# Kernel tuning notes

Measured on AMD Instinct MI355X. Metric: run time of the kernel, lower is better.

The kernel has to match this reference:

```python
import jax, jax.numpy as jnp
import numpy as np

EMBED_DIM = 2048
NUM_HEADS = 32
NUM_KV_HEADS = 8
HEAD_DIM = EMBED_DIM // NUM_HEADS  # 64
KV_DIM = NUM_KV_HEADS * HEAD_DIM   # 512


def setup_inputs() -> dict:
    key = jax.random.key(0)
    ks = jax.random.split(key, 5)
    B, S = 2, 2048
    scale = 0.02
    x = jax.random.normal(ks[0], (B, S, EMBED_DIM), dtype=jnp.float32)
    Wq = jax.random.normal(ks[1], (EMBED_DIM, EMBED_DIM), dtype=jnp.float32) * scale
    Wk = jax.random.normal(ks[2], (EMBED_DIM, KV_DIM), dtype=jnp.float32) * scale
    Wv = jax.random.normal(ks[3], (EMBED_DIM, KV_DIM), dtype=jnp.float32) * scale
    Wo = jax.random.normal(ks[4], (EMBED_DIM, EMBED_DIM), dtype=jnp.float32) * scale
    return {"x": x, "Wq": Wq, "Wk": Wk, "Wv": Wv, "Wo": Wo}


def reference(x, Wq, Wk, Wv, Wo):
    B, S, _ = x.shape
    g = NUM_HEADS // NUM_KV_HEADS  # queries per kv head
    # projections -> [B, H, S, D]
    q = (x @ Wq).reshape(B, S, NUM_HEADS, HEAD_DIM).transpose(0, 2, 1, 3)
    k = (x @ Wk).reshape(B, S, NUM_KV_HEADS, HEAD_DIM).transpose(0, 2, 1, 3)
    v = (x @ Wv).reshape(B, S, NUM_KV_HEADS, HEAD_DIM).transpose(0, 2, 1, 3)
    # GQA repeat_interleave on head dim
    k = jnp.repeat(k, g, axis=1)
    v = jnp.repeat(v, g, axis=1)
    scores = jnp.einsum('bhqd,bhkd->bhqk', q, k) / np.sqrt(HEAD_DIM).astype(np.float32)
    causal = jnp.tril(jnp.ones((S, S), dtype=bool))
    scores = jnp.where(causal, scores, jnp.finfo(x.dtype).min)
    attn = jax.nn.softmax(scores, axis=-1)
    out = jnp.einsum('bhqk,bhkd->bhqd', attn, v)  # [B, H, S, D]
    out = out.transpose(0, 2, 1, 3).reshape(B, S, EMBED_DIM)
    return out @ Wo
```

## Files before the change

### kernel.cpp

```cpp
#include <hip/hip_runtime.h>
#include <hip/hip_bf16.h>
#include <cstdint>
#include <type_traits>

#define EMBED 2048
#define SLEN 2048
#define NB 2
#define NHEADS 32
#define HDIM 64
#define KVDIM 512
#define MTOT (NB * SLEN)
#define NQKV (EMBED + 2 * KVDIM)

typedef __attribute__((ext_vector_type(8))) __bf16 bf16x8;
typedef __attribute__((ext_vector_type(4))) float f32x4;
typedef __attribute__((ext_vector_type(16))) float f32x16;

#define QSCALE 0.18033688011112042f

__device__ __forceinline__ ushort f2bf(float f) {
    union { float f; uint32_t u; } v; v.f = f;
    uint32_t r = (v.u + 0x7FFFu + ((v.u >> 16) & 1u)) >> 16;
    return (ushort)r;
}

__device__ __forceinline__ void gload_lds16(const ushort* g, ushort* l) {
    __builtin_amdgcn_global_load_lds(
        (const __attribute__((address_space(1))) void*)g,
        (__attribute__((address_space(3))) void*)l, 16, 0, 0);
}

__global__ __launch_bounds__(256) void k_prep(const float* __restrict__ x,
                                              const float* __restrict__ Wq,
                                              const float* __restrict__ Wk,
                                              const float* __restrict__ Wv,
                                              const float* __restrict__ Wo,
                                              ushort* __restrict__ xb,
                                              ushort* __restrict__ wt,
                                              ushort* __restrict__ wot) {
    const int tid = threadIdx.x;
    int bid = blockIdx.x;
    if (bid < 8192) {
        int i = bid * 256 + tid;
        float4 v = *(const float4*)(x + (size_t)i * 4);
        ushort4 o;
        o.x = f2bf(v.x); o.y = f2bf(v.y); o.z = f2bf(v.z); o.w = f2bf(v.w);
        *(ushort4*)(xb + (size_t)i * 4) = o;
        return;
    }
    bid -= 8192;
    const float* W; ushort* Wt; int N; float scale; int bx, by;
    if (bid < 4096)      { W = Wq; Wt = wt;                                   N = EMBED; scale = QSCALE; bx = bid & 63; by = bid >> 6; }
    else if (bid < 5120) { W = Wk; Wt = wt + (size_t)EMBED * EMBED;           N = KVDIM; scale = 1.f; int b2 = bid - 4096; bx = b2 & 15; by = b2 >> 4; }
    else if (bid < 6144) { W = Wv; Wt = wt + (size_t)(EMBED + KVDIM) * EMBED; N = KVDIM; scale = 1.f; int b2 = bid - 5120; bx = b2 & 15; by = b2 >> 4; }
    else                 { W = Wo; Wt = wot;                                  N = EMBED; scale = 1.f; int b2 = bid - 6144; bx = b2 & 63; by = b2 >> 6; }
    const int K = EMBED;
    __shared__ float tile[32][33];
    const int tx = tid & 31, ty = tid >> 5;
    const int xcol = bx * 32 + tx;
    const int y0 = by * 32;
    #pragma unroll
    for (int i = ty; i < 32; i += 8)
        tile[i][tx] = W[(size_t)(y0 + i) * N + xcol];
    __syncthreads();
    const int xo = y0 + tx;
    const int yo0 = bx * 32;
    #pragma unroll
    for (int i = ty; i < 32; i += 8)
        Wt[(size_t)(yo0 + i) * K + xo] = f2bf(tile[tx][i] * scale);
}

__global__ __launch_bounds__(256) void k_transpose_v(const ushort* __restrict__ V,
                                                     ushort* __restrict__ VT) {
    __shared__ ushort tile[64][65];
    const int tx = threadIdx.x, ty = threadIdx.y;
    const int x0 = blockIdx.x * 64;
    const int y0 = blockIdx.y * 64;
    #pragma unroll
    for (int i = ty; i < 64; i += 4)
        tile[i][tx] = V[(size_t)(y0 + i) * KVDIM + x0 + tx];
    __syncthreads();
    #pragma unroll
    for (int i = ty; i < 64; i += 4)
        VT[(size_t)(x0 + i) * MTOT + y0 + tx] = tile[tx][i];
}

__device__ __forceinline__ int2 xcd_swizzle(int gx, int gy) {
    const int nwg = gx * gy;
    int f = blockIdx.y * gx + blockIdx.x;
    const int cpx = nwg >> 3;
    f = (f & 7) * cpx + (f >> 3);
    return make_int2(f % gx, f / gx);
}

__global__ __launch_bounds__(256) void k_gemm_qkv(const ushort* __restrict__ A,
                                                  const ushort* __restrict__ Bt,
                                                  ushort* __restrict__ Qb,
                                                  ushort* __restrict__ Kb,
                                                  ushort* __restrict__ Vb) {
    __shared__ alignas(16) ushort As[2][128 * 32];
    __shared__ alignas(16) ushort Bs[2][128 * 32];

    const int tid = threadIdx.x;
    const int lane = tid & 63;
    const int w = tid >> 6;
    const int wr = w >> 1, wc = w & 1;
    const int l15 = lane & 15, g = lane >> 4;
    const int2 bxy = xcd_swizzle(NQKV / 128, MTOT / 128);
    const int n0 = bxy.x * 128;
    const int m0 = bxy.y * 128;
    const int K = EMBED;

    f32x4 acc[4][4] = {};

    const int c0 = tid, c1 = tid + 256;
    const int rA0 = c0 >> 2, sA0 = c0 & 3;
    const int rA1 = c1 >> 2, sA1 = c1 & 3;

    const ushort* pA0 = A + (size_t)(m0 + rA0) * K + sA0 * 8;
    const ushort* pA1 = A + (size_t)(m0 + rA1) * K + sA1 * 8;
    const ushort* pB0 = Bt + (size_t)(n0 + rA0) * K + sA0 * 8;
    const ushort* pB1 = Bt + (size_t)(n0 + rA1) * K + sA1 * 8;

    gload_lds16(pA0, &As[0][c0 * 8]);
    gload_lds16(pA1, &As[0][c1 * 8]);
    gload_lds16(pB0, &Bs[0][c0 * 8]);
    gload_lds16(pB1, &Bs[0][c1 * 8]);
    __syncthreads();

    int cur = 0;
    for (int k0 = 0; k0 < K; k0 += 32) {
        if (k0 + 32 < K) {
            gload_lds16(pA0 + k0 + 32, &As[cur ^ 1][c0 * 8]);
            gload_lds16(pA1 + k0 + 32, &As[cur ^ 1][c1 * 8]);
            gload_lds16(pB0 + k0 + 32, &Bs[cur ^ 1][c0 * 8]);
            gload_lds16(pB1 + k0 + 32, &Bs[cur ^ 1][c1 * 8]);
        }
        bf16x8 a[4], b[4];
        #pragma unroll
        for (int i = 0; i < 4; i++)
            a[i] = *(const bf16x8*)&As[cur][(wr * 64 + i * 16 + l15) * 32 + 8 * g];
        #pragma unroll
        for (int j = 0; j < 4; j++)
            b[j] = *(const bf16x8*)&Bs[cur][(wc * 64 + j * 16 + l15) * 32 + 8 * g];
        #pragma unroll
        for (int i = 0; i < 4; i++)
            #pragma unroll
            for (int j = 0; j < 4; j++)
                acc[i][j] = __builtin_amdgcn_mfma_f32_16x16x32_bf16(a[i], b[j], acc[i][j], 0, 0, 0);
        __syncthreads();
        cur ^= 1;
    }

    ushort* Cb; int Nout, cbase;
    if (n0 < EMBED)              { Cb = Qb; Nout = EMBED; cbase = n0; }
    else if (n0 < EMBED + KVDIM) { Cb = Kb; Nout = KVDIM; cbase = n0 - EMBED; }
    else                         { Cb = Vb; Nout = KVDIM; cbase = n0 - EMBED - KVDIM; }

    #pragma unroll
    for (int i = 0; i < 4; i++) {
        #pragma unroll
        for (int j = 0; j < 4; j++) {
            const int row = m0 + wr * 64 + i * 16 + g * 4;
            const int col = cbase + wc * 64 + j * 16 + l15;
            #pragma unroll
            for (int r = 0; r < 4; r++)
                Cb[(size_t)(row + r) * Nout + col] = f2bf(acc[i][j][r]);
        }
    }
}

template <typename OUT_T>
__global__ __launch_bounds__(256) void k_gemm_bt(const ushort* __restrict__ A,
                                                 const ushort* __restrict__ Bt,
                                                 OUT_T* __restrict__ C,
                                                 int M, int N, int K) {
    __shared__ alignas(16) ushort As[2][128 * 64];
    __shared__ alignas(16) ushort Bs[2][128 * 64];

    const int tid = threadIdx.x;
    const int lane = tid & 63;
    const int w = tid >> 6;
    const int wr = w >> 1, wc = w & 1;
    const int l15 = lane & 15, g = lane >> 4;
    const int2 bxy = xcd_swizzle(N / 128, M / 128);
    const int n0 = bxy.x * 128;
    const int m0 = bxy.y * 128;

    f32x4 acc[4][4] = {};

    const ushort* pA[4];
    const ushort* pB[4];
    #pragma unroll
    for (int t = 0; t < 4; t++) {
        const int c = tid + 256 * t;
        const int r = c >> 3, gr = c & 7;
        const int sg = gr ^ (r & 7);
        pA[t] = A + (size_t)(m0 + r) * K + sg * 8;
        pB[t] = Bt + (size_t)(n0 + r) * K + sg * 8;
    }

    #pragma unroll
    for (int t = 0; t < 4; t++) {
        gload_lds16(pA[t], &As[0][(tid + 256 * t) * 8]);
        gload_lds16(pB[t], &Bs[0][(tid + 256 * t) * 8]);
    }
    __syncthreads();

    int cur = 0;
    for (int k0 = 0; k0 < K; k0 += 64) {
        if (k0 + 64 < K) {
            #pragma unroll
            for (int t = 0; t < 4; t++) {
                gload_lds16(pA[t] + k0 + 64, &As[cur ^ 1][(tid + 256 * t) * 8]);
                gload_lds16(pB[t] + k0 + 64, &Bs[cur ^ 1][(tid + 256 * t) * 8]);
            }
        }
        #pragma unroll
        for (int kk = 0; kk < 2; kk++) {
            bf16x8 a[4], b[4];
            #pragma unroll
            for (int i = 0; i < 4; i++)
                a[i] = *(const bf16x8*)&As[cur][(wr * 64 + i * 16 + l15) * 64 +
                                                (((4 * kk + g) ^ (l15 & 7)) << 3)];
            #pragma unroll
            for (int j = 0; j < 4; j++)
                b[j] = *(const bf16x8*)&Bs[cur][(wc * 64 + j * 16 + l15) * 64 +
                                                (((4 * kk + g) ^ (l15 & 7)) << 3)];
            #pragma unroll
            for (int i = 0; i < 4; i++)
                #pragma unroll
                for (int j = 0; j < 4; j++)
                    acc[i][j] = __builtin_amdgcn_mfma_f32_16x16x32_bf16(a[i], b[j], acc[i][j], 0, 0, 0);
        }
        __syncthreads();
        cur ^= 1;
    }

    #pragma unroll
    for (int i = 0; i < 4; i++) {
        #pragma unroll
        for (int j = 0; j < 4; j++) {
            const int row = m0 + wr * 64 + i * 16 + g * 4;
            const int col = n0 + wc * 64 + j * 16 + l15;
            #pragma unroll
            for (int r = 0; r < 4; r++) {
                float val = acc[i][j][r];
                if constexpr (std::is_same<OUT_T, ushort>::value)
                    C[(size_t)(row + r) * N + col] = f2bf(val);
                else
                    C[(size_t)(row + r) * N + col] = val;
            }
        }
    }
}

__global__ __launch_bounds__(512, 4) void k_attn(const ushort* __restrict__ Qg,
                                                 const ushort* __restrict__ Kg,
                                                 const ushort* __restrict__ VTg,
                                                 ushort* __restrict__ Og) {
    __shared__ alignas(16) ushort Ks[2][64 * 64];
    __shared__ alignas(16) ushort Vs[2][64 * 64];

    const int tid = threadIdx.x;
    const int lane = tid & 63;
    const int wq = tid >> 6;
    const int l31 = lane & 31;
    const int hi = lane >> 5;

    const int flat = blockIdx.x + (blockIdx.y << 3) + (blockIdx.z << 8);
    const int lo = flat & 255, hv = flat >> 8;
    const int bi = hv ? (7 - (lo & 7)) : (lo & 7);
    const int h = lo >> 3;
    const int b = hv;
    const int kh = h >> 2;
    const size_t rowbase = (size_t)b * SLEN;

    const int q0 = bi * 256;
    const int qw0 = q0 + wq * 32;
    const int nt = (q0 >> 6) + 4;

    bf16x8 qf[4];
    {
        const ushort* qrow = Qg + (rowbase + qw0 + l31) * EMBED + h * HDIM;
        #pragma unroll
        for (int s = 0; s < 4; s++)
            qf[s] = *(const bf16x8*)(qrow + s * 16 + hi * 8);
    }

    const int srow = tid >> 3;
    const int sgr = tid & 7;
    const int woff = srow * 64 + ((sgr ^ (srow & 7)) << 3);
    const ushort* kgbase = Kg + (rowbase + srow) * KVDIM + kh * HDIM + sgr * 8;
    const ushort* vgbase = VTg + (size_t)(kh * HDIM + srow) * MTOT + b * SLEN + sgr * 8;

    {
        uint4 kr = *(const uint4*)kgbase;
        uint4 vr = *(const uint4*)vgbase;
        *(uint4*)&Ks[0][woff] = kr;
        *(uint4*)&Vs[0][woff] = vr;
    }
    __syncthreads();

    f32x16 oacc[2];
    #pragma unroll
    for (int d = 0; d < 2; d++)
        #pragma unroll
        for (int r = 0; r < 16; r++) oacc[d][r] = 0.f;
    float l_run = 0.f;

    int cur = 0;
    for (int kt = 0; kt < nt; ++kt) {
        const int k0 = kt * 64;
        const bool pref = (kt + 1 < nt);
        uint4 kr, vr;
        if (pref) {
            kr = *(const uint4*)(kgbase + (size_t)(k0 + 64) * KVDIM);
            vr = *(const uint4*)(vgbase + k0 + 64);
        }

        if (k0 <= qw0 + 31) {
            f32x16 sacc[2];
            #pragma unroll
            for (int st = 0; st < 2; st++)
                #pragma unroll
                for (int r = 0; r < 16; r++) sacc[st][r] = 0.f;
            __builtin_amdgcn_s_setprio(1);
            #pragma unroll
            for (int st = 0; st < 2; st++) {
                const int krow = st * 32 + l31;
                #pragma unroll
                for (int s = 0; s < 4; s++) {
                    bf16x8 af = *(const bf16x8*)&Ks[cur][krow * 64 + (((2 * s + hi) ^ (l31 & 7)) << 3)];
                    sacc[st] = __builtin_amdgcn_mfma_f32_32x32x16_bf16(af, qf[s], sacc[st], 0, 0, 0);
                }
            }
            __builtin_amdgcn_s_setprio(0);
            if (k0 + 63 > qw0) {
                const int q = qw0 + l31;
                #pragma unroll
                for (int st = 0; st < 2; st++)
                    #pragma unroll
                    for (int r = 0; r < 16; r++) {
                        int kpos = k0 + st * 32 + (r & 3) + 8 * (r >> 2) + 4 * hi;
                        if (kpos > q) sacc[st][r] = -1e30f;
                    }
            }
            float lsum = 0.f;
            #pragma unroll
            for (int st = 0; st < 2; st++)
                #pragma unroll
                for (int r = 0; r < 16; r++) {
                    float p = __builtin_amdgcn_exp2f(sacc[st][r]);
                    sacc[st][r] = p;
                    lsum += p;
                }
            lsum += __shfl_xor(lsum, 32);
            l_run += lsum;
            uint32_t pr[2][8];
            #pragma unroll
            for (int st = 0; st < 2; st++)
                #pragma unroll
                for (int k = 0; k < 8; k++) {
                    uint32_t d;
                    asm("v_cvt_pk_bf16_f32 %0, %1, %2"
                        : "=v"(d) : "v"(sacc[st][2 * k]), "v"(sacc[st][2 * k + 1]));
                    pr[st][k] = d;
                }
            #pragma unroll
            for (int c = 0; c < 2; c++) {
                #pragma unroll
                for (int tt = 0; tt < 2; tt++) {
                    const int pb = 4 * tt;
                    uint32_t w0 = pr[c][pb + 0], w2 = pr[c][pb + 2];
                    uint32_t w1 = pr[c][pb + 1], w3 = pr[c][pb + 3];
                    asm("v_permlane32_swap_b32 %0, %1" : "+v"(w0), "+v"(w2));
                    asm("v_permlane32_swap_b32 %0, %1" : "+v"(w1), "+v"(w3));
                    union { uint32_t u[4]; bf16x8 v; } pf;
                    pf.u[0] = w0; pf.u[1] = w1; pf.u[2] = w2; pf.u[3] = w3;
                    const int t = 2 * c + tt;
                    __builtin_amdgcn_s_setprio(1);
                    #pragma unroll
                    for (int dt = 0; dt < 2; dt++) {
                        const int vrow = dt * 32 + l31;
                        bf16x8 vf = *(const bf16x8*)&Vs[cur][vrow * 64 + (((2 * t + hi) ^ (l31 & 7)) << 3)];
                        oacc[dt] = __builtin_amdgcn_mfma_f32_32x32x16_bf16(pf.v, vf, oacc[dt], 0, 0, 0);
                    }
                    __builtin_amdgcn_s_setprio(0);
                }
            }
        }

        __syncthreads();
        if (pref) {
            *(uint4*)&Ks[cur ^ 1][woff] = kr;
            *(uint4*)&Vs[cur ^ 1][woff] = vr;
        }
        __syncthreads();
        cur ^= 1;
    }

    #pragma unroll
    for (int r = 0; r < 16; r++) {
        const int rr = (r & 3) + 8 * (r >> 2) + 4 * hi;
        float lr = __shfl(l_run, rr | (lane & 32));
        float inv = 1.f / lr;
        const size_t base = (rowbase + qw0 + rr) * EMBED + h * HDIM;
        Og[base + l31] = f2bf(oacc[0][r] * inv);
        Og[base + 32 + l31] = f2bf(oacc[1][r] * inv);
    }
}

#define WS_XB  ((size_t)0)
#define WS_QB  (WS_XB + (size_t)MTOT * EMBED)
#define WS_KB  (WS_QB + (size_t)MTOT * EMBED)
#define WS_VB  (WS_KB + (size_t)MTOT * KVDIM)
#define WS_WT  (WS_VB + (size_t)MTOT * KVDIM)
#define WS_WOT (WS_WT + (size_t)NQKV * EMBED)
#define WS_VT  WS_WT

extern "C" void kernel_launch(void* const* d_in, const int* in_sizes, int n_in,
                              void* d_out, int out_size, void* d_ws, size_t ws_size,
                              hipStream_t stream) {
    const float* x  = (const float*)d_in[0];
    const float* Wq = (const float*)d_in[1];
    const float* Wk = (const float*)d_in[2];
    const float* Wv = (const float*)d_in[3];
    const float* Wo = (const float*)d_in[4];
    float* out = (float*)d_out;
    ushort* ws = (ushort*)d_ws;

    k_prep<<<18432, 256, 0, stream>>>(x, Wq, Wk, Wv, Wo,
                                      ws + WS_XB, ws + WS_WT, ws + WS_WOT);

    k_gemm_qkv<<<dim3(NQKV / 128, MTOT / 128), 256, 0, stream>>>(
        ws + WS_XB, ws + WS_WT, ws + WS_QB, ws + WS_KB, ws + WS_VB);

    k_transpose_v<<<dim3(KVDIM / 64, MTOT / 64), dim3(64, 4), 0, stream>>>(
        ws + WS_VB, ws + WS_VT);

    k_attn<<<dim3(8, 32, 2), 512, 0, stream>>>(
        ws + WS_QB, ws + WS_KB, ws + WS_VT, ws + WS_XB);

    k_gemm_bt<float><<<dim3(EMBED / 128, MTOT / 128), 256, 0, stream>>>(
        ws + WS_XB, ws + WS_WOT, out, MTOT, EMBED, EMBED);
}
```

Baseline: 189.4 us.

## Split fused QKV GEMM into Q GEMM and a smaller-tile KV GEMM

Replaces the single QKV projection kernel (BK=32, 128x128 tiles) with two launches: the existing K=64-step bt GEMM for Q, and a new KV GEMM using 64x128 tiles with XOR-swizzled LDS and BK=64. K and V are written interleaved into one buffer with a 1024-element row stride, so the transpose and attention kernels now index through that stride. This aims to use the deeper-K, bank-conflict-free GEMM path and give the narrow KV projection more workgroups. The cost is an extra kernel launch and a less compact K layout for attention loads.

```diff
diff --git a/kernel.cpp b/kernel.cpp
--- a/kernel.cpp
+++ b/kernel.cpp
@@ -9,6 +9,7 @@
 #define NHEADS 32
 #define HDIM 64
 #define KVDIM 512
+#define KVSTRIDE 1024
 #define MTOT (NB * SLEN)
 #define NQKV (EMBED + 2 * KVDIM)
 
@@ -70,7 +71,7 @@
         Wt[(size_t)(yo0 + i) * K + xo] = f2bf(tile[tx][i] * scale);
 }
 
-__global__ __launch_bounds__(256) void k_transpose_v(const ushort* __restrict__ V,
+__global__ __launch_bounds__(256) void k_transpose_v(const ushort* __restrict__ KV,
                                                      ushort* __restrict__ VT) {
     __shared__ ushort tile[64][65];
     const int tx = threadIdx.x, ty = threadIdx.y;
@@ -78,7 +79,7 @@
     const int y0 = blockIdx.y * 64;
     #pragma unroll
     for (int i = ty; i < 64; i += 4)
-        tile[i][tx] = V[(size_t)(y0 + i) * KVDIM + x0 + tx];
+        tile[i][tx] = KV[(size_t)(y0 + i) * KVSTRIDE + KVDIM + x0 + tx];
     __syncthreads();
     #pragma unroll
     for (int i = ty; i < 64; i += 4)
@@ -91,83 +92,6 @@
     const int cpx = nwg >> 3;
     f = (f & 7) * cpx + (f >> 3);
     return make_int2(f % gx, f / gx);
-}
-
-__global__ __launch_bounds__(256) void k_gemm_qkv(const ushort* __restrict__ A,
-                                                  const ushort* __restrict__ Bt,
-                                                  ushort* __restrict__ Qb,
-                                                  ushort* __restrict__ Kb,
-                                                  ushort* __restrict__ Vb) {
-    __shared__ alignas(16) ushort As[2][128 * 32];
-    __shared__ alignas(16) ushort Bs[2][128 * 32];
-
-    const int tid = threadIdx.x;
-    const int lane = tid & 63;
-    const int w = tid >> 6;
-    const int wr = w >> 1, wc = w & 1;
-    const int l15 = lane & 15, g = lane >> 4;
-    const int2 bxy = xcd_swizzle(NQKV / 128, MTOT / 128);
-    const int n0 = bxy.x * 128;
-    const int m0 = bxy.y * 128;
-    const int K = EMBED;
-
-    f32x4 acc[4][4] = {};
-
-    const int c0 = tid, c1 = tid + 256;
-    const int rA0 = c0 >> 2, sA0 = c0 & 3;
-    const int rA1 = c1 >> 2, sA1 = c1 & 3;
-
-    const ushort* pA0 = A + (size_t)(m0 + rA0) * K + sA0 * 8;
-    const ushort* pA1 = A + (size_t)(m0 + rA1) * K + sA1 * 8;
-    const ushort* pB0 = Bt + (size_t)(n0 + rA0) * K + sA0 * 8;
-    const ushort* pB1 = Bt + (size_t)(n0 + rA1) * K + sA1 * 8;
-
-    gload_lds16(pA0, &As[0][c0 * 8]);
-    gload_lds16(pA1, &As[0][c1 * 8]);
-    gload_lds16(pB0, &Bs[0][c0 * 8]);
-    gload_lds16(pB1, &Bs[0][c1 * 8]);
-    __syncthreads();
-
-    int cur = 0;
-    for (int k0 = 0; k0 < K; k0 += 32) {
-        if (k0 + 32 < K) {
-            gload_lds16(pA0 + k0 + 32, &As[cur ^ 1][c0 * 8]);
-            gload_lds16(pA1 + k0 + 32, &As[cur ^ 1][c1 * 8]);
-            gload_lds16(pB0 + k0 + 32, &Bs[cur ^ 1][c0 * 8]);
-            gload_lds16(pB1 + k0 + 32, &Bs[cur ^ 1][c1 * 8]);
-        }
-        bf16x8 a[4], b[4];
-        #pragma unroll
-        for (int i = 0; i < 4; i++)
-            a[i] = *(const bf16x8*)&As[cur][(wr * 64 + i * 16 + l15) * 32 + 8 * g];
-        #pragma unroll
-        for (int j = 0; j < 4; j++)
-            b[j] = *(const bf16x8*)&Bs[cur][(wc * 64 + j * 16 + l15) * 32 + 8 * g];
-        #pragma unroll
-        for (int i = 0; i < 4; i++)
-            #pragma unroll
-            for (int j = 0; j < 4; j++)
-                acc[i][j] = __builtin_amdgcn_mfma_f32_16x16x32_bf16(a[i], b[j], acc[i][j], 0, 0, 0);
-        __syncthreads();
-        cur ^= 1;
-    }
-
-    ushort* Cb; int Nout, cbase;
-    if (n0 < EMBED)              { Cb = Qb; Nout = EMBED; cbase = n0; }
-    else if (n0 < EMBED + KVDIM) { Cb = Kb; Nout = KVDIM; cbase = n0 - EMBED; }
-    else                         { Cb = Vb; Nout = KVDIM; cbase = n0 - EMBED - KVDIM; }
-
-    #pragma unroll
-    for (int i = 0; i < 4; i++) {
-        #pragma unroll
-        for (int j = 0; j < 4; j++) {
-            const int row = m0 + wr * 64 + i * 16 + g * 4;
-            const int col = cbase + wc * 64 + j * 16 + l15;
-            #pragma unroll
-            for (int r = 0; r < 4; r++)
-                Cb[(size_t)(row + r) * Nout + col] = f2bf(acc[i][j][r]);
-        }
-    }
 }
 
 template <typename OUT_T>
@@ -255,8 +179,95 @@
     }
 }
 
+__global__ __launch_bounds__(256) void k_gemm_kv(const ushort* __restrict__ A,
+                                                 const ushort* __restrict__ Bt,
+                                                 ushort* __restrict__ C) {
+    __shared__ alignas(16) ushort As[2][64 * 64];
+    __shared__ alignas(16) ushort Bs[2][128 * 64];
+
+    const int tid = threadIdx.x;
+    const int lane = tid & 63;
+    const int w = tid >> 6;
+    const int wr = w >> 1, wc = w & 1;
+    const int l15 = lane & 15, g = lane >> 4;
+    const int2 bxy = xcd_swizzle(KVSTRIDE / 128, MTOT / 64);
+    const int n0 = bxy.x * 128;
+    const int m0 = bxy.y * 64;
+    const int K = EMBED;
+
+    f32x4 acc[2][4] = {};
+
+    const ushort* pA[2];
+    const ushort* pB[4];
+    #pragma unroll
+    for (int t = 0; t < 2; t++) {
+        const int c = tid + 256 * t;
+        const int r = c >> 3, gr = c & 7;
+        const int sg = gr ^ (r & 7);
+        pA[t] = A + (size_t)(m0 + r) * K + sg * 8;
+    }
+    #pragma unroll
+    for (int t = 0; t < 4; t++) {
+        const int c = tid + 256 * t;
+        const int r = c >> 3, gr = c & 7;
+        const int sg = gr ^ (r & 7);
+        pB[t] = Bt + (size_t)(n0 + r) * K + sg * 8;
+    }
+
+    #pragma unroll
+    for (int t = 0; t < 2; t++)
+        gload_lds16(pA[t], &As[0][(tid + 256 * t) * 8]);
+    #pragma unroll
+    for (int t = 0; t < 4; t++)
+        gload_lds16(pB[t], &Bs[0][(tid + 256 * t) * 8]);
+    __syncthreads();
+
+    int cur = 0;
+    for (int k0 = 0; k0 < K; k0 += 64) {
+        if (k0 + 64 < K) {
+            #pragma unroll
+            for (int t = 0; t < 2; t++)
+                gload_lds16(pA[t] + k0 + 64, &As[cur ^ 1][(tid + 256 * t) * 8]);
+            #pragma unroll
+            for (int t = 0; t < 4; t++)
+                gload_lds16(pB[t] + k0 + 64, &Bs[cur ^ 1][(tid + 256 * t) * 8]);
+        }
+        #pragma unroll
+        for (int kk = 0; kk < 2; kk++) {
+            bf16x8 a[2], b[4];
+            #pragma unroll
+            for (int i = 0; i < 2; i++)
+                a[i] = *(const bf16x8*)&As[cur][(wr * 32 + i * 16 + l15) * 64 +
+                                                (((4 * kk + g) ^ (l15 & 7)) << 3)];
+            #pragma unroll
+            for (int j = 0; j < 4; j++)
+                b[j] = *(const bf16x8*)&Bs[cur][(wc * 64 + j * 16 + l15) * 64 +
+                                                (((4 * kk + g) ^ (l15 & 7)) << 3)];
+            #pragma unroll
+            for (int i = 0; i < 2; i++)
+                #pragma unroll
+                for (int j = 0; j < 4; j++)
+                    acc[i][j] = __builtin_amdgcn_mfma_f32_16x16x32_bf16(a[i], b[j], acc[i][j], 0, 0, 0);
+        }
+        __syncthreads();
+        cur ^= 1;
+    }
+
+    #pragma unroll
+    for (int i = 0; i < 2; i++) {
+        #pragma unroll
+        for (int j = 0; j < 4; j++) {
+            const int row = m0 + wr * 32 + i * 16 + g * 4;
+            const int col = n0 + wc * 64 + j * 16 + l15;
+            #pragma unroll
+            for (int r = 0; r < 4; r++)
+                C[(size_t)(row + r) * KVSTRIDE + col] = f2bf(acc[i][j][r]);
+        }
+    }
+}
+
 __global__ __launch_bounds__(512, 4) void k_attn(const ushort* __restrict__ Qg,
-                                                 const ushort* __restrict__ Kg,
+                                                 const ushort* __restrict__ KVg,
                                                  const ushort* __restrict__ VTg,
                                                  ushort* __restrict__ Og) {
     __shared__ alignas(16) ushort Ks[2][64 * 64];
@@ -291,7 +302,7 @@
     const int srow = tid >> 3;
     const int sgr = tid & 7;
     const int woff = srow * 64 + ((sgr ^ (srow & 7)) << 3);
-    const ushort* kgbase = Kg + (rowbase + srow) * KVDIM + kh * HDIM + sgr * 8;
+    const ushort* kgbase = KVg + (rowbase + srow) * KVSTRIDE + kh * HDIM + sgr * 8;
     const ushort* vgbase = VTg + (size_t)(kh * HDIM + srow) * MTOT + b * SLEN + sgr * 8;
 
     {
@@ -315,7 +326,7 @@
         const bool pref = (kt + 1 < nt);
         uint4 kr, vr;
         if (pref) {
-            kr = *(const uint4*)(kgbase + (size_t)(k0 + 64) * KVDIM);
+            kr = *(const uint4*)(kgbase + (size_t)(k0 + 64) * KVSTRIDE);
             vr = *(const uint4*)(vgbase + k0 + 64);
         }
 
@@ -413,9 +424,8 @@
 
 #define WS_XB  ((size_t)0)
 #define WS_QB  (WS_XB + (size_t)MTOT * EMBED)
-#define WS_KB  (WS_QB + (size_t)MTOT * EMBED)
-#define WS_VB  (WS_KB + (size_t)MTOT * KVDIM)
-#define WS_WT  (WS_VB + (size_t)MTOT * KVDIM)
+#define WS_KVB (WS_QB + (size_t)MTOT * EMBED)
+#define WS_WT  (WS_KVB + (size_t)MTOT * KVSTRIDE)
 #define WS_WOT (WS_WT + (size_t)NQKV * EMBED)
 #define WS_VT  WS_WT
 
@@ -433,14 +443,17 @@
     k_prep<<<18432, 256, 0, stream>>>(x, Wq, Wk, Wv, Wo,
                                       ws + WS_XB, ws + WS_WT, ws + WS_WOT);
 
-    k_gemm_qkv<<<dim3(NQKV / 128, MTOT / 128), 256, 0, stream>>>(
-        ws + WS_XB, ws + WS_WT, ws + WS_QB, ws + WS_KB, ws + WS_VB);
+    k_gemm_bt<ushort><<<dim3(EMBED / 128, MTOT / 128), 256, 0, stream>>>(
+        ws + WS_XB, ws + WS_WT, ws + WS_QB, MTOT, EMBED, EMBED);
+
+    k_gemm_kv<<<dim3(KVSTRIDE / 128, MTOT / 64), 256, 0, stream>>>(
+        ws + WS_XB, ws + WS_WT + (size_t)EMBED * EMBED, ws + WS_KVB);
 
     k_transpose_v<<<dim3(KVDIM / 64, MTOT / 64), dim3(64, 4), 0, stream>>>(
-        ws + WS_VB, ws + WS_VT);
+        ws + WS_KVB, ws + WS_VT);
 
     k_attn<<<dim3(8, 32, 2), 512, 0, stream>>>(
-        ws + WS_QB, ws + WS_KB, ws + WS_VT, ws + WS_XB);
+        ws + WS_QB, ws + WS_KVB, ws + WS_VT, ws + WS_XB);
 
     k_gemm_bt<float><<<dim3(EMBED / 128, MTOT / 128), 256, 0, stream>>>(
         ws + WS_XB, ws + WS_WOT, out, MTOT, EMBED, EMBED);
```

After: 191.2 us. Within noise of the previous version (+0.9%).
